# Kernel tuning notes

Hardware: AMD Instinct MI355X
Metric: run time of the kernel (lower is better)

## Reference

```python
import jax, jax.numpy as jnp
import numpy as np

HIDDEN = 512
ANN = 512


def setup_inputs() -> dict:
    key = jax.random.key(0)
    k1, k2, k3, k4, k5, k6 = jax.random.split(key, 6)
    B, S = 32, 4096
    prev_hidden_state = jax.random.normal(k1, (B, HIDDEN), dtype=jnp.float32)
    annotations = jax.random.normal(k2, (B, S, ANN), dtype=jnp.float32)
    in_dim = HIDDEN + ANN
    # Kaiming-uniform-ish init like torch Linear
    lim1 = 1.0 / np.sqrt(in_dim)
    W1 = jax.random.uniform(k3, (in_dim, HIDDEN), dtype=jnp.float32, minval=-lim1, maxval=lim1)
    b1 = jax.random.uniform(k4, (HIDDEN,), dtype=jnp.float32, minval=-lim1, maxval=lim1)
    lim2 = 1.0 / np.sqrt(HIDDEN)
    W2 = jax.random.uniform(k5, (HIDDEN, 1), dtype=jnp.float32, minval=-lim2, maxval=lim2)
    b2 = jax.random.uniform(k6, (1,), dtype=jnp.float32, minval=-lim2, maxval=lim2)
    return {"prev_hidden_state": prev_hidden_state, "annotations": annotations,
            "W1": W1, "b1": b1, "W2": W2, "b2": b2}


def reference(prev_hidden_state, annotations, W1, b1, W2, b2):
    # Split W1 so we never materialize the [B,S,hidden+ann] concat:
    # concat([h_rep, ann]) @ W1 == h @ W1[:H] + ann @ W1[H:]
    W1_h, W1_a = W1[:HIDDEN], W1[HIDDEN:]
    # [B,1,H] + [B,S,H] -> [B,S,H]
    pre = prev_hidden_state @ W1_h  # [B,H]
    hidden = jnp.tanh(pre[:, None, :] + jnp.einsum('bsa,ah->bsh', annotations, W1_a) + b1)
    score = jnp.einsum('bsh,h->bs', hidden, W2[:, 0]) + b2[0]  # [B,S]
    alpha = jax.nn.softmax(score, axis=1)  # legacy F.softmax default dim=1
    # alpha.bmm(annotations): [B,1,S] @ [B,S,A] -> [B,1,A]
    context = jnp.einsum('bs,bsa->ba', alpha, annotations)[:, None, :]
    return context
```

## Files before the change

kernel.cpp:

```cpp
#include <hip/hip_runtime.h>

#define HID 512
#define SEQ 4096
#define NB 32
#define BS 64
#define NSB 16
#define CPB 4
#define CH 514

typedef __attribute__((ext_vector_type(8))) __bf16 bf16x8;
typedef __attribute__((ext_vector_type(4))) __bf16 bf16x4;
typedef __attribute__((ext_vector_type(16))) float f32x16;
typedef __attribute__((ext_vector_type(4))) float f32x4;

__device__ __forceinline__ float tanh_fast(float v) {
    float e = __expf(2.f * v);
    return 1.f - __fdividef(2.f, e + 1.f);
}

__global__ void build_w1af(const float* __restrict__ W1,
                           unsigned short* __restrict__ w1af) {
    __shared__ float tile[64][65];
    int t = threadIdx.x;
    int lane = t & 63;
    int r4 = t >> 6;
    int k0 = blockIdx.x * 64;
    int h0 = blockIdx.y * 64;
#pragma unroll
    for (int i = 0; i < 16; ++i) {
        int r = i * 4 + r4;
        tile[r][lane] = W1[(size_t)(HID + k0 + r) * HID + h0 + lane];
    }
    __syncthreads();
#pragma unroll
    for (int i = 0; i < 16; ++i) {
        int hr = i * 4 + r4;
        int h = h0 + hr, k = k0 + lane;
        __bf16 bv = (__bf16)tile[lane][hr];
        int ht = h >> 5, hl = h & 31;
        int ks = k >> 4, g = (k >> 3) & 1, j = k & 7;
        size_t off = (((size_t)ht * 32 + ks) * 64 + g * 32 + hl) * 8 + j;
        w1af[off] = *(unsigned short*)&bv;
    }
}

__global__ void pre_partial(const float* __restrict__ prev,
                            const float* __restrict__ W1,
                            float* __restrict__ pre_part) {
    __shared__ float pl[128];
    int kc = blockIdx.x;
    int b  = blockIdx.y;
    int t  = threadIdx.x;
    if (t < 128) pl[t] = prev[b * HID + kc * 128 + t];
    __syncthreads();
    int h0 = 2 * t;
    float ax = 0.f, ay = 0.f;
    for (int k = 0; k < 128; ++k) {
        float pv = pl[k];
        float2 wv = *(const float2*)(W1 + (size_t)(kc * 128 + k) * HID + h0);
        ax += pv * wv.x;
        ay += pv * wv.y;
    }
    float* dst = pre_part + ((size_t)b * 4 + kc) * HID + h0;
    dst[0] = ax; dst[1] = ay;
}

__global__ __launch_bounds__(256, 2)
void score_ctx(const float* __restrict__ ann,
               const unsigned short* __restrict__ w1af,
               const float* __restrict__ pre_part,
               const float* __restrict__ b1,
               const float* __restrict__ W2,
               float* __restrict__ cout) {
    __shared__ unsigned short buf[BS * 512];
    __shared__ float pre_lds[512];
    __shared__ float w2_lds[512];
    __shared__ float red[4][64];

    const int sb = blockIdx.x, b = blockIdx.y;
    const int t = threadIdx.x;
    const int wv = t >> 6;
    const int lane = t & 63;
    const int sl = lane & 31;
    const int g = lane >> 5;

#pragma unroll
    for (int j = 0; j < 2; ++j) {
        int h = t + j * 256;
        float pp = b1[h];
#pragma unroll
        for (int kc = 0; kc < 4; ++kc)
            pp += pre_part[((size_t)b * 4 + kc) * HID + h];
        pre_lds[h] = pp;
        w2_lds[h] = W2[h];
    }

    const float* abase0 = ann + ((size_t)b * SEQ + (size_t)sb * (CPB * BS)) * 512;

    float m_run = -3.0e38f, d_run = 0.f;
    float ctxa = 0.f, ctxb = 0.f;

    const unsigned short* wb0 = w1af + (size_t)(4 * wv) * 16384 + (size_t)lane * 8;
    const unsigned short* wb1 = wb0 + 16384;
    const unsigned short* wb2 = wb0 + 32768;
    const unsigned short* wb3 = wb0 + 49152;
    const unsigned swz = (unsigned)(sl & 7) << 4;
    const unsigned rb0 = (unsigned)(( 0 + sl) * 1024 + g * 16);
    const unsigned rb1 = (unsigned)((32 + sl) * 1024 + g * 16);

#pragma unroll 1
    for (int c = 0; c < CPB; ++c) {
        __syncthreads();

        const float* ab = abase0 + (size_t)c * BS * 512;
#pragma unroll 8
        for (int i = 0; i < 32; ++i) {
            int flat4 = t + i * 256;
            int row = flat4 >> 7, c4 = flat4 & 127;
            f32x4 f = __builtin_nontemporal_load((const f32x4*)(ab) + flat4);
            bf16x4 pk;
            pk[0] = (__bf16)f[0]; pk[1] = (__bf16)f[1];
            pk[2] = (__bf16)f[2]; pk[3] = (__bf16)f[3];
            unsigned boff = ((unsigned)(row * 1024 + c4 * 8)) ^ ((unsigned)(row & 7) << 4);
            *(bf16x4*)((char*)buf + boff) = pk;
        }
        __syncthreads();

        f32x16 c00, c01, c10, c11, c20, c21, c30, c31;
#pragma unroll
        for (int r = 0; r < 16; ++r) {
            c00[r] = 0.f; c01[r] = 0.f; c10[r] = 0.f; c11[r] = 0.f;
            c20[r] = 0.f; c21[r] = 0.f; c30[r] = 0.f; c31[r] = 0.f;
        }
#pragma unroll 2
        for (int ks = 0; ks < 32; ++ks) {
            bf16x8 A0 = *(const bf16x8*)(wb0 + ks * 512);
            bf16x8 A1 = *(const bf16x8*)(wb1 + ks * 512);
            bf16x8 A2 = *(const bf16x8*)(wb2 + ks * 512);
            bf16x8 A3 = *(const bf16x8*)(wb3 + ks * 512);
            unsigned kb = (unsigned)ks * 32u;
            bf16x8 B0 = *(const bf16x8*)((const char*)buf + ((rb0 + kb) ^ swz));
            bf16x8 B1 = *(const bf16x8*)((const char*)buf + ((rb1 + kb) ^ swz));
            c00 = __builtin_amdgcn_mfma_f32_32x32x16_bf16(A0, B0, c00, 0, 0, 0);
            c01 = __builtin_amdgcn_mfma_f32_32x32x16_bf16(A0, B1, c01, 0, 0, 0);
            c10 = __builtin_amdgcn_mfma_f32_32x32x16_bf16(A1, B0, c10, 0, 0, 0);
            c11 = __builtin_amdgcn_mfma_f32_32x32x16_bf16(A1, B1, c11, 0, 0, 0);
            c20 = __builtin_amdgcn_mfma_f32_32x32x16_bf16(A2, B0, c20, 0, 0, 0);
            c21 = __builtin_amdgcn_mfma_f32_32x32x16_bf16(A2, B1, c21, 0, 0, 0);
            c30 = __builtin_amdgcn_mfma_f32_32x32x16_bf16(A3, B0, c30, 0, 0, 0);
            c31 = __builtin_amdgcn_mfma_f32_32x32x16_bf16(A3, B1, c31, 0, 0, 0);
        }

        float sp0 = 0.f, sp1 = 0.f;
#pragma unroll
        for (int r = 0; r < 16; ++r) {
            int hl = (r & 3) + 8 * (r >> 2) + 4 * g;
            int h0 = wv * 128 + hl;
            float p0 = pre_lds[h0],      w0 = w2_lds[h0];
            float p1 = pre_lds[h0 + 32], w1 = w2_lds[h0 + 32];
            float p2 = pre_lds[h0 + 64], w2v = w2_lds[h0 + 64];
            float p3 = pre_lds[h0 + 96], w3 = w2_lds[h0 + 96];
            sp0 += w0 * tanh_fast(c00[r] + p0) + w1 * tanh_fast(c10[r] + p1)
                 + w2v * tanh_fast(c20[r] + p2) + w3 * tanh_fast(c30[r] + p3);
            sp1 += w0 * tanh_fast(c01[r] + p0) + w1 * tanh_fast(c11[r] + p1)
                 + w2v * tanh_fast(c21[r] + p2) + w3 * tanh_fast(c31[r] + p3);
        }
        sp0 += __shfl_xor(sp0, 32);
        sp1 += __shfl_xor(sp1, 32);
        if (lane < 32) { red[wv][sl] = sp0; red[wv][32 + sl] = sp1; }
        __syncthreads();

        float sc = red[0][lane] + red[1][lane] + red[2][lane] + red[3][lane];
        float m = sc;
#pragma unroll
        for (int off = 32; off; off >>= 1) m = fmaxf(m, __shfl_xor(m, off));
        float p = __expf(sc - m);
        float d = p;
#pragma unroll
        for (int off = 32; off; off >>= 1) d += __shfl_xor(d, off);

        float m_new = fmaxf(m_run, m);
        float so = __expf(m_run - m_new), s_c = __expf(m - m_new);
        d_run = d_run * so + d * s_c;

        float na = 0.f, nb = 0.f;
#pragma unroll 8
        for (int s = 0; s < BS; ++s) {
            float ps = __shfl(p, s);
            unsigned boff = ((unsigned)(s * 1024 + 4 * t)) ^ ((unsigned)(s & 7) << 4);
            unsigned u = *(const unsigned*)((const char*)buf + boff);
            na += ps * __uint_as_float(u << 16);
            nb += ps * __uint_as_float(u & 0xFFFF0000u);
        }
        ctxa = ctxa * so + na * s_c;
        ctxb = ctxb * so + nb * s_c;
        m_run = m_new;
    }

    float* cb = cout + ((size_t)b * NSB + sb) * CH;
    cb[2 + 2 * t]     = ctxa;
    cb[2 + 2 * t + 1] = ctxb;
    if (t == 0) { cb[0] = m_run; cb[1] = d_run; }
}

__global__ void finalize_ctx(const float* __restrict__ cout,
                             float* __restrict__ out) {
    int b = blockIdx.x, t = threadIdx.x;
    float ms[NSB];
    float M = -3.0e38f;
#pragma unroll
    for (int s = 0; s < NSB; ++s) {
        ms[s] = cout[((size_t)b * NSB + s) * CH];
        M = fmaxf(M, ms[s]);
    }
    float D = 0.f, val = 0.f;
#pragma unroll
    for (int s = 0; s < NSB; ++s) {
        const float* cb = cout + ((size_t)b * NSB + s) * CH;
        float e = __expf(ms[s] - M);
        D += e * cb[1];
        val += e * cb[2 + t];
    }
    out[(size_t)b * 512 + t] = val / D;
}

extern "C" void kernel_launch(void* const* d_in, const int* in_sizes, int n_in,
                              void* d_out, int out_size, void* d_ws, size_t ws_size,
                              hipStream_t stream) {
    (void)in_sizes; (void)n_in; (void)out_size; (void)ws_size;
    const float* prev = (const float*)d_in[0];
    const float* ann  = (const float*)d_in[1];
    const float* W1   = (const float*)d_in[2];
    const float* b1   = (const float*)d_in[3];
    const float* W2   = (const float*)d_in[4];
    float* out = (float*)d_out;

    char* ws = (char*)d_ws;
    unsigned short* w1af = (unsigned short*)ws;
    float* pre_part = (float*)(ws + 524288);
    float* cout     = (float*)(ws + 524288 + 262144);

    build_w1af<<<dim3(8, 8), dim3(256), 0, stream>>>(W1, w1af);
    pre_partial<<<dim3(4, NB), dim3(256), 0, stream>>>(prev, W1, pre_part);
    score_ctx<<<dim3(NSB, NB), dim3(256), 0, stream>>>(ann, w1af, pre_part, b1, W2, cout);
    finalize_ctx<<<dim3(NB), dim3(512), 0, stream>>>(cout, out);
}
```

Measured before the change: 140.4 us.

## Halve sequence tile to 32 rows and double blocks for higher occupancy

Each block now stages 32 annotation rows per chunk instead of 64, uses four MFMA accumulators instead of eight, and the grid doubles to 32 sequence blocks per batch. Launch bounds are raised to 4 blocks per CU, and the reduction and softmax shuffles are adjusted to 32 rows. The intent is to cut registers and LDS per block so more waves can hide memory and MFMA latency. In exchange, every bf16 W1 fragment fetched from global or L2 is reused across half as many rows, roughly doubling weight traffic. The annotation load also drops its nontemporal hint, and finalize merges twice as many partials.

Result: slower. 211.8 us (+50.9%).

```diff
diff --git a/kernel.cpp b/kernel.cpp
--- a/kernel.cpp
+++ b/kernel.cpp
@@ -3,8 +3,8 @@
 #define HID 512
 #define SEQ 4096
 #define NB 32
-#define BS 64
-#define NSB 16
+#define BS 32
+#define NSB 32
 #define CPB 4
 #define CH 514
 
@@ -65,17 +65,17 @@
     dst[0] = ax; dst[1] = ay;
 }
 
-__global__ __launch_bounds__(256, 2)
+__global__ __launch_bounds__(256, 4)
 void score_ctx(const float* __restrict__ ann,
                const unsigned short* __restrict__ w1af,
                const float* __restrict__ pre_part,
                const float* __restrict__ b1,
                const float* __restrict__ W2,
                float* __restrict__ cout) {
-    __shared__ unsigned short buf[BS * 512];
+    __shared__ unsigned short ann_lds[BS * 512];
     __shared__ float pre_lds[512];
     __shared__ float w2_lds[512];
-    __shared__ float red[4][64];
+    __shared__ float red[4][32];
 
     const int sb = blockIdx.x, b = blockIdx.y;
     const int t = threadIdx.x;
@@ -105,8 +105,7 @@
     const unsigned short* wb2 = wb0 + 32768;
     const unsigned short* wb3 = wb0 + 49152;
     const unsigned swz = (unsigned)(sl & 7) << 4;
-    const unsigned rb0 = (unsigned)(( 0 + sl) * 1024 + g * 16);
-    const unsigned rb1 = (unsigned)((32 + sl) * 1024 + g * 16);
+    const unsigned rb0 = (unsigned)(sl * 1024 + g * 16);
 
 #pragma unroll 1
     for (int c = 0; c < CPB; ++c) {
@@ -114,70 +113,56 @@
 
         const float* ab = abase0 + (size_t)c * BS * 512;
 #pragma unroll 8
-        for (int i = 0; i < 32; ++i) {
-            int flat4 = t + i * 256;
-            int row = flat4 >> 7, c4 = flat4 & 127;
-            f32x4 f = __builtin_nontemporal_load((const f32x4*)(ab) + flat4);
+        for (int i = 0; i < 16; ++i) {
+            int idx = t + i * 256;
+            int row = idx >> 7, c4 = idx & 127;
+            f32x4 f = *((const f32x4*)(ab) + idx);
             bf16x4 pk;
             pk[0] = (__bf16)f[0]; pk[1] = (__bf16)f[1];
             pk[2] = (__bf16)f[2]; pk[3] = (__bf16)f[3];
             unsigned boff = ((unsigned)(row * 1024 + c4 * 8)) ^ ((unsigned)(row & 7) << 4);
-            *(bf16x4*)((char*)buf + boff) = pk;
+            *(bf16x4*)((char*)ann_lds + boff) = pk;
         }
         __syncthreads();
 
-        f32x16 c00, c01, c10, c11, c20, c21, c30, c31;
-#pragma unroll
-        for (int r = 0; r < 16; ++r) {
-            c00[r] = 0.f; c01[r] = 0.f; c10[r] = 0.f; c11[r] = 0.f;
-            c20[r] = 0.f; c21[r] = 0.f; c30[r] = 0.f; c31[r] = 0.f;
-        }
+        f32x16 c0, c1, c2, c3;
+#pragma unroll
+        for (int r = 0; r < 16; ++r) { c0[r] = 0.f; c1[r] = 0.f; c2[r] = 0.f; c3[r] = 0.f; }
 #pragma unroll 2
         for (int ks = 0; ks < 32; ++ks) {
             bf16x8 A0 = *(const bf16x8*)(wb0 + ks * 512);
             bf16x8 A1 = *(const bf16x8*)(wb1 + ks * 512);
             bf16x8 A2 = *(const bf16x8*)(wb2 + ks * 512);
             bf16x8 A3 = *(const bf16x8*)(wb3 + ks * 512);
-            unsigned kb = (unsigned)ks * 32u;
-            bf16x8 B0 = *(const bf16x8*)((const char*)buf + ((rb0 + kb) ^ swz));
-            bf16x8 B1 = *(const bf16x8*)((const char*)buf + ((rb1 + kb) ^ swz));
-            c00 = __builtin_amdgcn_mfma_f32_32x32x16_bf16(A0, B0, c00, 0, 0, 0);
-            c01 = __builtin_amdgcn_mfma_f32_32x32x16_bf16(A0, B1, c01, 0, 0, 0);
-            c10 = __builtin_amdgcn_mfma_f32_32x32x16_bf16(A1, B0, c10, 0, 0, 0);
-            c11 = __builtin_amdgcn_mfma_f32_32x32x16_bf16(A1, B1, c11, 0, 0, 0);
-            c20 = __builtin_amdgcn_mfma_f32_32x32x16_bf16(A2, B0, c20, 0, 0, 0);
-            c21 = __builtin_amdgcn_mfma_f32_32x32x16_bf16(A2, B1, c21, 0, 0, 0);
-            c30 = __builtin_amdgcn_mfma_f32_32x32x16_bf16(A3, B0, c30, 0, 0, 0);
-            c31 = __builtin_amdgcn_mfma_f32_32x32x16_bf16(A3, B1, c31, 0, 0, 0);
-        }
-
-        float sp0 = 0.f, sp1 = 0.f;
+            bf16x8 B0 = *(const bf16x8*)((const char*)ann_lds + ((rb0 + (unsigned)ks * 32u) ^ swz));
+            c0 = __builtin_amdgcn_mfma_f32_32x32x16_bf16(A0, B0, c0, 0, 0, 0);
+            c1 = __builtin_amdgcn_mfma_f32_32x32x16_bf16(A1, B0, c1, 0, 0, 0);
+            c2 = __builtin_amdgcn_mfma_f32_32x32x16_bf16(A2, B0, c2, 0, 0, 0);
+            c3 = __builtin_amdgcn_mfma_f32_32x32x16_bf16(A3, B0, c3, 0, 0, 0);
+        }
+
+        float sp = 0.f;
 #pragma unroll
         for (int r = 0; r < 16; ++r) {
             int hl = (r & 3) + 8 * (r >> 2) + 4 * g;
             int h0 = wv * 128 + hl;
-            float p0 = pre_lds[h0],      w0 = w2_lds[h0];
-            float p1 = pre_lds[h0 + 32], w1 = w2_lds[h0 + 32];
-            float p2 = pre_lds[h0 + 64], w2v = w2_lds[h0 + 64];
-            float p3 = pre_lds[h0 + 96], w3 = w2_lds[h0 + 96];
-            sp0 += w0 * tanh_fast(c00[r] + p0) + w1 * tanh_fast(c10[r] + p1)
-                 + w2v * tanh_fast(c20[r] + p2) + w3 * tanh_fast(c30[r] + p3);
-            sp1 += w0 * tanh_fast(c01[r] + p0) + w1 * tanh_fast(c11[r] + p1)
-                 + w2v * tanh_fast(c21[r] + p2) + w3 * tanh_fast(c31[r] + p3);
-        }
-        sp0 += __shfl_xor(sp0, 32);
-        sp1 += __shfl_xor(sp1, 32);
-        if (lane < 32) { red[wv][sl] = sp0; red[wv][32 + sl] = sp1; }
+            sp += w2_lds[h0]      * tanh_fast(c0[r] + pre_lds[h0])
+                + w2_lds[h0 + 32] * tanh_fast(c1[r] + pre_lds[h0 + 32])
+                + w2_lds[h0 + 64] * tanh_fast(c2[r] + pre_lds[h0 + 64])
+                + w2_lds[h0 + 96] * tanh_fast(c3[r] + pre_lds[h0 + 96]);
+        }
+        sp += __shfl_xor(sp, 32);
+        if (lane < 32) red[wv][sl] = sp;
         __syncthreads();
 
-        float sc = red[0][lane] + red[1][lane] + red[2][lane] + red[3][lane];
+        float sc = red[0][sl] + red[1][sl] + red[2][sl] + red[3][sl];
         float m = sc;
 #pragma unroll
-        for (int off = 32; off; off >>= 1) m = fmaxf(m, __shfl_xor(m, off));
+        for (int off = 16; off; off >>= 1) m = fmaxf(m, __shfl_xor(m, off));
         float p = __expf(sc - m);
         float d = p;
 #pragma unroll
-        for (int off = 32; off; off >>= 1) d += __shfl_xor(d, off);
+        for (int off = 16; off; off >>= 1) d += __shfl_xor(d, off);
 
         float m_new = fmaxf(m_run, m);
         float so = __expf(m_run - m_new), s_c = __expf(m - m_new);
@@ -188,7 +173,7 @@
         for (int s = 0; s < BS; ++s) {
             float ps = __shfl(p, s);
             unsigned boff = ((unsigned)(s * 1024 + 4 * t)) ^ ((unsigned)(s & 7) << 4);
-            unsigned u = *(const unsigned*)((const char*)buf + boff);
+            unsigned u = *(const unsigned*)((const char*)ann_lds + boff);
             na += ps * __uint_as_float(u << 16);
             nb += ps * __uint_as_float(u & 0xFFFF0000u);
         }
@@ -206,18 +191,13 @@
 __global__ void finalize_ctx(const float* __restrict__ cout,
                              float* __restrict__ out) {
     int b = blockIdx.x, t = threadIdx.x;
-    float ms[NSB];
     float M = -3.0e38f;
-#pragma unroll
-    for (int s = 0; s < NSB; ++s) {
-        ms[s] = cout[((size_t)b * NSB + s) * CH];
-        M = fmaxf(M, ms[s]);
-    }
+    for (int s = 0; s < NSB; ++s)
+        M = fmaxf(M, cout[((size_t)b * NSB + s) * CH]);
     float D = 0.f, val = 0.f;
-#pragma unroll
     for (int s = 0; s < NSB; ++s) {
         const float* cb = cout + ((size_t)b * NSB + s) * CH;
-        float e = __expf(ms[s] - M);
+        float e = __expf(cb[0] - M);
         D += e * cb[1];
         val += e * cb[2 + t];
     }
```

## Warp-specialize score_ctx with producer waves double-buffering annotation chunks

Applied to the files above, without the earlier changes.

Splits each block into 4 consumer waves doing MFMA/tanh/softmax/context and 4 producer waves that prefetch the next 64-row annotation chunk into registers, convert it to bf16 and write it into a second LDS buffer. The aim is to overlap global loads with compute instead of serializing load then compute per chunk. Grid halves to 8 sequence blocks per batch with 8 chunks each. This doubles LDS use to about 128KB per block and holds 32 f32x4 registers per producer thread, which likely limits occupancy to one block per CU and leaves fewer blocks (256) to fill the device.

New measurement: 387.2 us. 176% more time.

```diff
diff --git a/kernel.cpp b/kernel.cpp
--- a/kernel.cpp
+++ b/kernel.cpp
@@ -4,8 +4,8 @@
 #define SEQ 4096
 #define NB 32
 #define BS 64
-#define NSB 16
-#define CPB 4
+#define NSB 8
+#define CPB 8
 #define CH 514
 
 typedef __attribute__((ext_vector_type(8))) __bf16 bf16x8;
@@ -65,14 +65,15 @@
     dst[0] = ax; dst[1] = ay;
 }
 
-__global__ __launch_bounds__(256, 2)
+__global__ __launch_bounds__(512, 2)
 void score_ctx(const float* __restrict__ ann,
                const unsigned short* __restrict__ w1af,
                const float* __restrict__ pre_part,
                const float* __restrict__ b1,
                const float* __restrict__ W2,
                float* __restrict__ cout) {
-    __shared__ unsigned short buf[BS * 512];
+    __shared__ unsigned short bufA[BS * 512];
+    __shared__ unsigned short bufB[BS * 512];
     __shared__ float pre_lds[512];
     __shared__ float w2_lds[512];
     __shared__ float red[4][64];
@@ -83,27 +84,43 @@
     const int lane = t & 63;
     const int sl = lane & 31;
     const int g = lane >> 5;
-
-#pragma unroll
-    for (int j = 0; j < 2; ++j) {
-        int h = t + j * 256;
-        float pp = b1[h];
-#pragma unroll
-        for (int kc = 0; kc < 4; ++kc)
-            pp += pre_part[((size_t)b * 4 + kc) * HID + h];
-        pre_lds[h] = pp;
-        w2_lds[h] = W2[h];
-    }
+    const int pt = t - 256;
 
     const float* abase0 = ann + ((size_t)b * SEQ + (size_t)sb * (CPB * BS)) * 512;
+
+    f32x4 sf[32];
+
+    if (wv >= 4) {
+#pragma unroll
+        for (int i = 0; i < 32; ++i)
+            sf[i] = __builtin_nontemporal_load((const f32x4*)(abase0) + pt + i * 256);
+#pragma unroll
+        for (int i = 0; i < 32; ++i) {
+            int idx = pt + i * 256;
+            int row = idx >> 7, c4 = idx & 127;
+            bf16x4 pk;
+            pk[0] = (__bf16)sf[i][0]; pk[1] = (__bf16)sf[i][1];
+            pk[2] = (__bf16)sf[i][2]; pk[3] = (__bf16)sf[i][3];
+            unsigned boff = ((unsigned)(row * 1024 + c4 * 8)) ^ ((unsigned)(row & 7) << 4);
+            *(bf16x4*)((char*)bufA + boff) = pk;
+        }
+    } else {
+#pragma unroll
+        for (int j = 0; j < 2; ++j) {
+            int h = t + j * 256;
+            float pp = b1[h];
+#pragma unroll
+            for (int kc = 0; kc < 4; ++kc)
+                pp += pre_part[((size_t)b * 4 + kc) * HID + h];
+            pre_lds[h] = pp;
+            w2_lds[h] = W2[h];
+        }
+    }
 
     float m_run = -3.0e38f, d_run = 0.f;
     float ctxa = 0.f, ctxb = 0.f;
 
-    const unsigned short* wb0 = w1af + (size_t)(4 * wv) * 16384 + (size_t)lane * 8;
-    const unsigned short* wb1 = wb0 + 16384;
-    const unsigned short* wb2 = wb0 + 32768;
-    const unsigned short* wb3 = wb0 + 49152;
+    const unsigned short* wbp = w1af + (size_t)(4 * wv) * 16384 + (size_t)lane * 8;
     const unsigned swz = (unsigned)(sl & 7) << 4;
     const unsigned rb0 = (unsigned)(( 0 + sl) * 1024 + g * 16);
     const unsigned rb1 = (unsigned)((32 + sl) * 1024 + g * 16);
@@ -111,96 +128,106 @@
 #pragma unroll 1
     for (int c = 0; c < CPB; ++c) {
         __syncthreads();
-
-        const float* ab = abase0 + (size_t)c * BS * 512;
+        unsigned short* cur = (c & 1) ? bufB : bufA;
+        unsigned short* nxt = (c & 1) ? bufA : bufB;
+
+        if (wv < 4) {
+            f32x16 a0, a1, a2, a3, b0a, b1a, b2a, b3a;
+#pragma unroll
+            for (int r = 0; r < 16; ++r) {
+                a0[r] = 0.f; a1[r] = 0.f; a2[r] = 0.f; a3[r] = 0.f;
+                b0a[r] = 0.f; b1a[r] = 0.f; b2a[r] = 0.f; b3a[r] = 0.f;
+            }
+#pragma unroll 2
+            for (int ks = 0; ks < 32; ++ks) {
+                bf16x8 A0 = *(const bf16x8*)(wbp +     0 + ks * 512);
+                bf16x8 A1 = *(const bf16x8*)(wbp + 16384 + ks * 512);
+                bf16x8 A2 = *(const bf16x8*)(wbp + 32768 + ks * 512);
+                bf16x8 A3 = *(const bf16x8*)(wbp + 49152 + ks * 512);
+                unsigned kb = (unsigned)ks * 32u;
+                bf16x8 B0 = *(const bf16x8*)((const char*)cur + ((rb0 + kb) ^ swz));
+                bf16x8 B1 = *(const bf16x8*)((const char*)cur + ((rb1 + kb) ^ swz));
+                a0  = __builtin_amdgcn_mfma_f32_32x32x16_bf16(A0, B0, a0, 0, 0, 0);
+                b0a = __builtin_amdgcn_mfma_f32_32x32x16_bf16(A0, B1, b0a, 0, 0, 0);
+                a1  = __builtin_amdgcn_mfma_f32_32x32x16_bf16(A1, B0, a1, 0, 0, 0);
+                b1a = __builtin_amdgcn_mfma_f32_32x32x16_bf16(A1, B1, b1a, 0, 0, 0);
+                a2  = __builtin_amdgcn_mfma_f32_32x32x16_bf16(A2, B0, a2, 0, 0, 0);
+                b2a = __builtin_amdgcn_mfma_f32_32x32x16_bf16(A2, B1, b2a, 0, 0, 0);
+                a3  = __builtin_amdgcn_mfma_f32_32x32x16_bf16(A3, B0, a3, 0, 0, 0);
+                b3a = __builtin_amdgcn_mfma_f32_32x32x16_bf16(A3, B1, b3a, 0, 0, 0);
+            }
+            float sp0 = 0.f, sp1 = 0.f;
+#pragma unroll
+            for (int r = 0; r < 16; ++r) {
+                int hl = (r & 3) + 8 * (r >> 2) + 4 * g;
+                int h0 = wv * 128 + hl;
+                float p0 = pre_lds[h0],      w0 = w2_lds[h0];
+                float p1 = pre_lds[h0 + 32], w1 = w2_lds[h0 + 32];
+                float p2 = pre_lds[h0 + 64], w2v = w2_lds[h0 + 64];
+                float p3 = pre_lds[h0 + 96], w3 = w2_lds[h0 + 96];
+                sp0 += w0 * tanh_fast(a0[r] + p0)  + w1 * tanh_fast(a1[r] + p1)
+                     + w2v * tanh_fast(a2[r] + p2) + w3 * tanh_fast(a3[r] + p3);
+                sp1 += w0 * tanh_fast(b0a[r] + p0)  + w1 * tanh_fast(b1a[r] + p1)
+                     + w2v * tanh_fast(b2a[r] + p2) + w3 * tanh_fast(b3a[r] + p3);
+            }
+            sp0 += __shfl_xor(sp0, 32);
+            sp1 += __shfl_xor(sp1, 32);
+            if (lane < 32) { red[wv][sl] = sp0; red[wv][32 + sl] = sp1; }
+        } else if (c < CPB - 1) {
+            const float* ab = abase0 + (size_t)(c + 1) * BS * 512;
+#pragma unroll
+            for (int i = 0; i < 32; ++i)
+                sf[i] = __builtin_nontemporal_load((const f32x4*)(ab) + pt + i * 256);
+        }
+
+        __syncthreads();
+
+        if (wv < 4) {
+            float sc = red[0][lane] + red[1][lane] + red[2][lane] + red[3][lane];
+            float m = sc;
+#pragma unroll
+            for (int off = 32; off; off >>= 1) m = fmaxf(m, __shfl_xor(m, off));
+            float p = __expf(sc - m);
+            float d = p;
+#pragma unroll
+            for (int off = 32; off; off >>= 1) d += __shfl_xor(d, off);
+
+            float m_new = fmaxf(m_run, m);
+            float so = __expf(m_run - m_new), s_c = __expf(m - m_new);
+            d_run = d_run * so + d * s_c;
+
+            float na = 0.f, nb = 0.f;
 #pragma unroll 8
-        for (int i = 0; i < 32; ++i) {
-            int flat4 = t + i * 256;
-            int row = flat4 >> 7, c4 = flat4 & 127;
-            f32x4 f = __builtin_nontemporal_load((const f32x4*)(ab) + flat4);
-            bf16x4 pk;
-            pk[0] = (__bf16)f[0]; pk[1] = (__bf16)f[1];
-            pk[2] = (__bf16)f[2]; pk[3] = (__bf16)f[3];
-            unsigned boff = ((unsigned)(row * 1024 + c4 * 8)) ^ ((unsigned)(row & 7) << 4);
-            *(bf16x4*)((char*)buf + boff) = pk;
-        }
-        __syncthreads();
-
-        f32x16 c00, c01, c10, c11, c20, c21, c30, c31;
-#pragma unroll
-        for (int r = 0; r < 16; ++r) {
-            c00[r] = 0.f; c01[r] = 0.f; c10[r] = 0.f; c11[r] = 0.f;
-            c20[r] = 0.f; c21[r] = 0.f; c30[r] = 0.f; c31[r] = 0.f;
-        }
-#pragma unroll 2
-        for (int ks = 0; ks < 32; ++ks) {
-            bf16x8 A0 = *(const bf16x8*)(wb0 + ks * 512);
-            bf16x8 A1 = *(const bf16x8*)(wb1 + ks * 512);
-            bf16x8 A2 = *(const bf16x8*)(wb2 + ks * 512);
-            bf16x8 A3 = *(const bf16x8*)(wb3 + ks * 512);
-            unsigned kb = (unsigned)ks * 32u;
-            bf16x8 B0 = *(const bf16x8*)((const char*)buf + ((rb0 + kb) ^ swz));
-            bf16x8 B1 = *(const bf16x8*)((const char*)buf + ((rb1 + kb) ^ swz));
-            c00 = __builtin_amdgcn_mfma_f32_32x32x16_bf16(A0, B0, c00, 0, 0, 0);
-            c01 = __builtin_amdgcn_mfma_f32_32x32x16_bf16(A0, B1, c01, 0, 0, 0);
-            c10 = __builtin_amdgcn_mfma_f32_32x32x16_bf16(A1, B0, c10, 0, 0, 0);
-            c11 = __builtin_amdgcn_mfma_f32_32x32x16_bf16(A1, B1, c11, 0, 0, 0);
-            c20 = __builtin_amdgcn_mfma_f32_32x32x16_bf16(A2, B0, c20, 0, 0, 0);
-            c21 = __builtin_amdgcn_mfma_f32_32x32x16_bf16(A2, B1, c21, 0, 0, 0);
-            c30 = __builtin_amdgcn_mfma_f32_32x32x16_bf16(A3, B0, c30, 0, 0, 0);
-            c31 = __builtin_amdgcn_mfma_f32_32x32x16_bf16(A3, B1, c31, 0, 0, 0);
-        }
-
-        float sp0 = 0.f, sp1 = 0.f;
-#pragma unroll
-        for (int r = 0; r < 16; ++r) {
-            int hl = (r & 3) + 8 * (r >> 2) + 4 * g;
-            int h0 = wv * 128 + hl;
-            float p0 = pre_lds[h0],      w0 = w2_lds[h0];
-            float p1 = pre_lds[h0 + 32], w1 = w2_lds[h0 + 32];
-            float p2 = pre_lds[h0 + 64], w2v = w2_lds[h0 + 64];
-            float p3 = pre_lds[h0 + 96], w3 = w2_lds[h0 + 96];
-            sp0 += w0 * tanh_fast(c00[r] + p0) + w1 * tanh_fast(c10[r] + p1)
-                 + w2v * tanh_fast(c20[r] + p2) + w3 * tanh_fast(c30[r] + p3);
-            sp1 += w0 * tanh_fast(c01[r] + p0) + w1 * tanh_fast(c11[r] + p1)
-                 + w2v * tanh_fast(c21[r] + p2) + w3 * tanh_fast(c31[r] + p3);
-        }
-        sp0 += __shfl_xor(sp0, 32);
-        sp1 += __shfl_xor(sp1, 32);
-        if (lane < 32) { red[wv][sl] = sp0; red[wv][32 + sl] = sp1; }
-        __syncthreads();
-
-        float sc = red[0][lane] + red[1][lane] + red[2][lane] + red[3][lane];
-        float m = sc;
-#pragma unroll
-        for (int off = 32; off; off >>= 1) m = fmaxf(m, __shfl_xor(m, off));
-        float p = __expf(sc - m);
-        float d = p;
-#pragma unroll
-        for (int off = 32; off; off >>= 1) d += __shfl_xor(d, off);
-
-        float m_new = fmaxf(m_run, m);
-        float so = __expf(m_run - m_new), s_c = __expf(m - m_new);
-        d_run = d_run * so + d * s_c;
-
-        float na = 0.f, nb = 0.f;
-#pragma unroll 8
-        for (int s = 0; s < BS; ++s) {
-            float ps = __shfl(p, s);
-            unsigned boff = ((unsigned)(s * 1024 + 4 * t)) ^ ((unsigned)(s & 7) << 4);
-            unsigned u = *(const unsigned*)((const char*)buf + boff);
-            na += ps * __uint_as_float(u << 16);
-            nb += ps * __uint_as_float(u & 0xFFFF0000u);
-        }
-        ctxa = ctxa * so + na * s_c;
-        ctxb = ctxb * so + nb * s_c;
-        m_run = m_new;
-    }
-
-    float* cb = cout + ((size_t)b * NSB + sb) * CH;
-    cb[2 + 2 * t]     = ctxa;
-    cb[2 + 2 * t + 1] = ctxb;
-    if (t == 0) { cb[0] = m_run; cb[1] = d_run; }
+            for (int s = 0; s < BS; ++s) {
+                float ps = __shfl(p, s);
+                unsigned boff = ((unsigned)(s * 1024 + 4 * t)) ^ ((unsigned)(s & 7) << 4);
+                unsigned u = *(const unsigned*)((const char*)cur + boff);
+                na += ps * __uint_as_float(u << 16);
+                nb += ps * __uint_as_float(u & 0xFFFF0000u);
+            }
+            ctxa = ctxa * so + na * s_c;
+            ctxb = ctxb * so + nb * s_c;
+            m_run = m_new;
+        } else if (c < CPB - 1) {
+#pragma unroll
+            for (int i = 0; i < 32; ++i) {
+                int idx = pt + i * 256;
+                int row = idx >> 7, c4 = idx & 127;
+                bf16x4 pk;
+                pk[0] = (__bf16)sf[i][0]; pk[1] = (__bf16)sf[i][1];
+                pk[2] = (__bf16)sf[i][2]; pk[3] = (__bf16)sf[i][3];
+                unsigned boff = ((unsigned)(row * 1024 + c4 * 8)) ^ ((unsigned)(row & 7) << 4);
+                *(bf16x4*)((char*)nxt + boff) = pk;
+            }
+        }
+    }
+
+    if (t < 256) {
+        float* cb = cout + ((size_t)b * NSB + sb) * CH;
+        cb[2 + 2 * t]     = ctxa;
+        cb[2 + 2 * t + 1] = ctxb;
+        if (t == 0) { cb[0] = m_run; cb[1] = d_run; }
+    }
 }
 
 __global__ void finalize_ctx(const float* __restrict__ cout,
@@ -242,6 +269,6 @@
 
     build_w1af<<<dim3(8, 8), dim3(256), 0, stream>>>(W1, w1af);
     pre_partial<<<dim3(4, NB), dim3(256), 0, stream>>>(prev, W1, pre_part);
-    score_ctx<<<dim3(NSB, NB), dim3(256), 0, stream>>>(ann, w1af, pre_part, b1, W2, cout);
+    score_ctx<<<dim3(NSB, NB), dim3(512), 0, stream>>>(ann, w1af, pre_part, b1, W2, cout);
     finalize_ctx<<<dim3(NB), dim3(512), 0, stream>>>(cout, out);
 }
```
